# Kernel tuning notes

Hardware: AMD Instinct MI355X
Metric: run time of the kernel (lower is better)

Reference implementation:

```python
import jax, jax.numpy as jnp
import numpy as np

N_NODES = 100000
N_EDGES = 1600000
NFEAT, NHID, NCLASS = 64, 128, 32


def _glorot(key, shape):
    fan_in, fan_out = shape[0], shape[1]
    lim = np.sqrt(6.0 / (fan_in + fan_out))
    return jax.random.uniform(key, shape, jnp.float32, -lim, lim)


def setup_inputs() -> dict:
    key = jax.random.key(0)
    ks = jax.random.split(key, 12)
    x = jax.random.normal(ks[0], (N_NODES, NFEAT), jnp.float32)
    edge_idx = jax.random.randint(ks[1], (2, N_EDGES), 0, N_NODES, jnp.int64)
    edge_weight = jax.random.uniform(ks[2], (N_EDGES,), jnp.float32)
    return {
        "x": x,
        "edge_idx": edge_idx,
        "edge_weight": edge_weight,
        # SAGEConv 1: out = mean_agg(x) @ Wl1 + b1 + x @ Wr1
        "Wl1": _glorot(ks[3], (NFEAT, NHID)),
        "Wr1": _glorot(ks[4], (NFEAT, NHID)),
        "b1": jnp.zeros((NHID,), jnp.float32),
        # SAGEConv 2
        "Wl2": _glorot(ks[5], (NHID, NHID)),
        "Wr2": _glorot(ks[6], (NHID, NHID)),
        "b2": jnp.zeros((NHID,), jnp.float32),
        # fc head: Linear(nhid, nclass) -> Linear(nclass, 1)
        "Wfc1": _glorot(ks[7], (NHID, NCLASS)),
        "bfc1": jnp.zeros((NCLASS,), jnp.float32),
        "Wfc2": _glorot(ks[8], (NCLASS, 1)),
        "bfc2": jnp.zeros((1,), jnp.float32),
    }


def _sage_conv(x, src, dst, Wl, Wr, b, n_nodes):
    # mean aggregation of source features at destination nodes
    msg_sum = jax.ops.segment_sum(x[src], dst, num_segments=n_nodes)  # [N, d]
    deg = jax.ops.segment_sum(jnp.ones((src.shape[0], 1), x.dtype), dst,
                              num_segments=n_nodes)                    # [N, 1]
    mean = msg_sum / jnp.maximum(deg, 1.0)
    return mean @ Wl + b + x @ Wr


def reference(x, edge_idx, edge_weight, Wl1, Wr1, b1, Wl2, Wr2, b2,
              Wfc1, bfc1, Wfc2, bfc2):
    n_nodes = x.shape[0]
    src, dst = edge_idx[0], edge_idx[1]
    # dropout is identity in eval mode (training=False)
    h = _sage_conv(x, src, dst, Wl1, Wr1, b1, n_nodes)   # [N, nhid]
    h = _sage_conv(h, src, dst, Wl2, Wr2, b2, n_nodes)   # [N, nhid]
    h = h @ Wfc1 + bfc1                                   # [N, nclass]
    out = h @ Wfc2 + bfc2                                 # [N, 1]
    return out
```

## Files before the change

kernel.cpp:

```cpp
#include <hip/hip_runtime.h>

#define S_NODES 512
#define S_SHIFT 9
#define CAP     10240
#define CHUNK   8192

__global__ void weights_kernel(const float* __restrict__ Wl1, const float* __restrict__ Wr1,
                               const float* __restrict__ b1,
                               const float* __restrict__ Wl2, const float* __restrict__ Wr2,
                               const float* __restrict__ b2,
                               const float* __restrict__ Wfc1, const float* __restrict__ bfc1,
                               const float* __restrict__ Wfc2, const float* __restrict__ bfc2,
                               float* __restrict__ wbuf) {
    __shared__ float u[128], vl2[128], vr2[128], w2[32];
    int t = threadIdx.x;
    if (t < 32) w2[t] = Wfc2[t];
    __syncthreads();
    {
        float s = 0.f;
        for (int k = 0; k < 32; ++k) s += Wfc1[t * 32 + k] * w2[k];
        u[t] = s;
    }
    __syncthreads();
    {
        float a = 0.f, b = 0.f;
        for (int k = 0; k < 128; ++k) {
            a += Wl2[t * 128 + k] * u[k];
            b += Wr2[t * 128 + k] * u[k];
        }
        vl2[t] = a; vr2[t] = b;
    }
    __syncthreads();
    if (t < 64) {
        float wa = 0.f, wb = 0.f, wc = 0.f;
        for (int j = 0; j < 128; ++j) {
            float l1 = Wl1[t * 128 + j], r1 = Wr1[t * 128 + j];
            wc += l1 * vl2[j];
            wb += l1 * vr2[j] + r1 * vl2[j];
            wa += r1 * vr2[j];
        }
        wbuf[t] = wa; wbuf[64 + t] = wb; wbuf[128 + t] = wc;
    }
    if (t == 0) {
        float c0 = bfc2[0], c1 = 0.f;
        for (int j = 0; j < 128; ++j) {
            c0 += b1[j] * vr2[j] + b2[j] * u[j];
            c1 += b1[j] * vl2[j];
        }
        for (int k = 0; k < 32; ++k) c0 += bfc1[k] * w2[k];
        wbuf[192] = c0; wbuf[193] = c1;
    }
}

__global__ void dots_kernel(const float* __restrict__ x, const float* __restrict__ wbuf,
                            float* __restrict__ ga, float2* __restrict__ gbc, int N) {
    int tid = threadIdx.x, lane = tid & 63;
    int node = blockIdx.x * 4 + (tid >> 6);
    if (node >= N) return;
    float v = x[(size_t)node * 64 + lane];
    float a = v * wbuf[lane];
    float b = v * wbuf[64 + lane];
    float c = v * wbuf[128 + lane];
    for (int off = 32; off > 0; off >>= 1) {
        a += __shfl_down(a, off);
        b += __shfl_down(b, off);
        c += __shfl_down(c, off);
    }
    if (lane == 0) { ga[node] = a; gbc[node] = make_float2(b, c); }
}

__global__ void scatter_bucket_kernel(const int* __restrict__ src, const int* __restrict__ dst,
                                      int E, int B, int* __restrict__ cursor,
                                      unsigned* __restrict__ bucket) {
    __shared__ unsigned pk[CHUNK];
    __shared__ unsigned char bn[CHUNK];
    __shared__ int hist[256], lbase[256], lcur[256];
    int t = threadIdx.x;
    int e0 = blockIdx.x * CHUNK;
    int cnt = E - e0; if (cnt > CHUNK) cnt = CHUNK;
    hist[t] = 0; lcur[t] = 0;
    __syncthreads();
    for (int i = t; i < cnt; i += 256) {
        int s = src[e0 + i], d = dst[e0 + i];
        int b = d >> S_SHIFT;
        pk[i] = ((unsigned)s << S_SHIFT) | (unsigned)(d & (S_NODES - 1));
        bn[i] = (unsigned char)b;
        atomicAdd(&hist[b], 1);
    }
    __syncthreads();
    if (t < B && hist[t] > 0) lbase[t] = atomicAdd(&cursor[t], hist[t]);
    __syncthreads();
    for (int i = t; i < cnt; i += 256) {
        int b = bn[i];
        int off = atomicAdd(&lcur[b], 1);
        bucket[(size_t)b * CAP + (unsigned)(lbase[b] + off)] = pk[i];
    }
}

__global__ void aggA_kernel(const unsigned* __restrict__ bucket, const int* __restrict__ cursor,
                            const float2* __restrict__ gbc, const float* __restrict__ ga,
                            const float* __restrict__ wbuf,
                            float* __restrict__ q, float* __restrict__ t1,
                            float* __restrict__ inv, int N) {
    __shared__ float aB[S_NODES], aC[S_NODES];
    __shared__ int cnt[S_NODES];
    int t = threadIdx.x, b = blockIdx.x;
    for (int i = t; i < S_NODES; i += 256) { aB[i] = 0.f; aC[i] = 0.f; cnt[i] = 0; }
    __syncthreads();
    int n = cursor[b];
    const unsigned* bp = bucket + (size_t)b * CAP;
    for (int i = t; i < n; i += 256) {
        unsigned u = bp[i];
        float2 g = gbc[u >> S_SHIFT];
        int dl = u & (S_NODES - 1);
        atomicAdd(&aB[dl], g.x);
        atomicAdd(&aC[dl], g.y);
        atomicAdd(&cnt[dl], 1);
    }
    __syncthreads();
    float c0 = wbuf[192], c1 = wbuf[193];
    int base = b << S_SHIFT;
    for (int i = t; i < S_NODES; i += 256) {
        int node = base + i;
        if (node < N) {
            int d = cnt[i];
            float iv = 1.0f / ((d > 0) ? (float)d : 1.0f);
            inv[node] = iv;
            q[node]   = iv * aC[i];
            t1[node]  = ga[node] + iv * aB[i] + c0 + (d > 0 ? c1 : 0.f);
        }
    }
}

__global__ void aggB_kernel(const unsigned* __restrict__ bucket, const int* __restrict__ cursor,
                            const float* __restrict__ q, const float* __restrict__ t1,
                            const float* __restrict__ inv, float* __restrict__ out, int N) {
    __shared__ float a2[S_NODES];
    int t = threadIdx.x, b = blockIdx.x;
    for (int i = t; i < S_NODES; i += 256) a2[i] = 0.f;
    __syncthreads();
    int n = cursor[b];
    const unsigned* bp = bucket + (size_t)b * CAP;
    for (int i = t; i < n; i += 256) {
        unsigned u = bp[i];
        atomicAdd(&a2[u & (S_NODES - 1)], q[u >> S_SHIFT]);
    }
    __syncthreads();
    int base = b << S_SHIFT;
    for (int i = t; i < S_NODES; i += 256) {
        int node = base + i;
        if (node < N) out[node] = t1[node] + inv[node] * a2[i];
    }
}

extern "C" void kernel_launch(void* const* d_in, const int* in_sizes, int n_in,
                              void* d_out, int out_size, void* d_ws, size_t ws_size,
                              hipStream_t stream) {
    const float* x    = (const float*)d_in[0];
    const int*   eidx = (const int*)d_in[1];
    const float* Wl1  = (const float*)d_in[3];
    const float* Wr1  = (const float*)d_in[4];
    const float* b1   = (const float*)d_in[5];
    const float* Wl2  = (const float*)d_in[6];
    const float* Wr2  = (const float*)d_in[7];
    const float* b2   = (const float*)d_in[8];
    const float* Wfc1 = (const float*)d_in[9];
    const float* bfc1 = (const float*)d_in[10];
    const float* Wfc2 = (const float*)d_in[11];
    const float* bfc2 = (const float*)d_in[12];

    const int N = in_sizes[0] / 64;
    const int E = in_sizes[2];
    const int* src = eidx;
    const int* dst = eidx + E;
    const int B = (N + S_NODES - 1) / S_NODES;

    char* ws = (char*)d_ws;
    int*      cursor = (int*)(ws);
    float*    wbuf   = (float*)(ws + 1024);
    float*    ga     = (float*)(ws + 2048);
    float*    q      = (float*)(ws + 2048 + (size_t)N * 4);
    float*    t1     = (float*)(ws + 2048 + (size_t)N * 8);
    float*    inv    = (float*)(ws + 2048 + (size_t)N * 12);
    float2*   gbc    = (float2*)(ws + 2048 + (size_t)N * 16);
    unsigned* bucket = (unsigned*)(ws + 2048 + (size_t)N * 24);

    hipMemsetAsync(cursor, 0, 1024, stream);

    weights_kernel<<<1, 128, 0, stream>>>(Wl1, Wr1, b1, Wl2, Wr2, b2,
                                          Wfc1, bfc1, Wfc2, bfc2, wbuf);

    dots_kernel<<<(N + 3) / 4, 256, 0, stream>>>(x, wbuf, ga, gbc, N);

    scatter_bucket_kernel<<<(E + CHUNK - 1) / CHUNK, 256, 0, stream>>>(src, dst, E, B,
                                                                       cursor, bucket);

    aggA_kernel<<<B, 256, 0, stream>>>(bucket, cursor, gbc, ga, wbuf, q, t1, inv, N);
    aggB_kernel<<<B, 256, 0, stream>>>(bucket, cursor, q, t1, inv, (float*)d_out, N);
}
```

Baseline: 193.2 us.

## Fuse weight folding, node dots and edge bucketing into one heterogeneous kernel

Merges the weight-collapse, per-node dot-product and edge-scatter kernels into one launch. Some blocks bucket edges while the rest each recompute the folded weight vectors redundantly and then do the dots with a grid-stride loop. This removes two launches and the serial dependency on the single-block weight kernel. The aggregation kernels move to 1024 threads per block to raise parallelism per bucket, and the scatter uses 512 threads. The cost is redundant weight computation in 192 blocks and larger blocks competing for resources.

Result: no change. 196.2 us (+1.5%).

```diff
diff --git a/kernel.cpp b/kernel.cpp
--- a/kernel.cpp
+++ b/kernel.cpp
@@ -4,152 +4,154 @@
 #define S_SHIFT 9
 #define CAP     10240
 #define CHUNK   8192
-
-__global__ void weights_kernel(const float* __restrict__ Wl1, const float* __restrict__ Wr1,
-                               const float* __restrict__ b1,
-                               const float* __restrict__ Wl2, const float* __restrict__ Wr2,
-                               const float* __restrict__ b2,
-                               const float* __restrict__ Wfc1, const float* __restrict__ bfc1,
-                               const float* __restrict__ Wfc2, const float* __restrict__ bfc2,
-                               float* __restrict__ wbuf) {
-    __shared__ float u[128], vl2[128], vr2[128], w2[32];
-    int t = threadIdx.x;
-    if (t < 32) w2[t] = Wfc2[t];
-    __syncthreads();
-    {
-        float s = 0.f;
-        for (int k = 0; k < 32; ++k) s += Wfc1[t * 32 + k] * w2[k];
-        u[t] = s;
-    }
-    __syncthreads();
-    {
-        float a = 0.f, b = 0.f;
-        for (int k = 0; k < 128; ++k) {
-            a += Wl2[t * 128 + k] * u[k];
-            b += Wr2[t * 128 + k] * u[k];
-        }
-        vl2[t] = a; vr2[t] = b;
-    }
-    __syncthreads();
-    if (t < 64) {
-        float wa = 0.f, wb = 0.f, wc = 0.f;
-        for (int j = 0; j < 128; ++j) {
-            float l1 = Wl1[t * 128 + j], r1 = Wr1[t * 128 + j];
-            wc += l1 * vl2[j];
-            wb += l1 * vr2[j] + r1 * vl2[j];
-            wa += r1 * vr2[j];
-        }
-        wbuf[t] = wa; wbuf[64 + t] = wb; wbuf[128 + t] = wc;
-    }
-    if (t == 0) {
-        float c0 = bfc2[0], c1 = 0.f;
-        for (int j = 0; j < 128; ++j) {
-            c0 += b1[j] * vr2[j] + b2[j] * u[j];
-            c1 += b1[j] * vl2[j];
-        }
-        for (int k = 0; k < 32; ++k) c0 += bfc1[k] * w2[k];
-        wbuf[192] = c0; wbuf[193] = c1;
-    }
-}
-
-__global__ void dots_kernel(const float* __restrict__ x, const float* __restrict__ wbuf,
-                            float* __restrict__ ga, float2* __restrict__ gbc, int N) {
-    int tid = threadIdx.x, lane = tid & 63;
-    int node = blockIdx.x * 4 + (tid >> 6);
-    if (node >= N) return;
-    float v = x[(size_t)node * 64 + lane];
-    float a = v * wbuf[lane];
-    float b = v * wbuf[64 + lane];
-    float c = v * wbuf[128 + lane];
-    for (int off = 32; off > 0; off >>= 1) {
-        a += __shfl_down(a, off);
-        b += __shfl_down(b, off);
-        c += __shfl_down(c, off);
-    }
-    if (lane == 0) { ga[node] = a; gbc[node] = make_float2(b, c); }
-}
-
-__global__ void scatter_bucket_kernel(const int* __restrict__ src, const int* __restrict__ dst,
-                                      int E, int B, int* __restrict__ cursor,
-                                      unsigned* __restrict__ bucket) {
+#define FTH     512
+#define NDOTS   192
+
+__global__ __launch_bounds__(512) void fused_kernel(
+    const float* __restrict__ x,
+    const int* __restrict__ src, const int* __restrict__ dst, int E, int B, int nscat,
+    int* __restrict__ cursor, unsigned* __restrict__ bucket,
+    const float* __restrict__ Wl1, const float* __restrict__ Wr1, const float* __restrict__ b1,
+    const float* __restrict__ Wl2, const float* __restrict__ Wr2, const float* __restrict__ b2,
+    const float* __restrict__ Wfc1, const float* __restrict__ bfc1,
+    const float* __restrict__ Wfc2, const float* __restrict__ bfc2,
+    float* __restrict__ ga, float2* __restrict__ gbc, float* __restrict__ c01, int N)
+{
     __shared__ unsigned pk[CHUNK];
     __shared__ unsigned char bn[CHUNK];
     __shared__ int hist[256], lbase[256], lcur[256];
+    __shared__ float u[128], vl2[128], vr2[128], w2[32], wv[192];
+
     int t = threadIdx.x;
-    int e0 = blockIdx.x * CHUNK;
-    int cnt = E - e0; if (cnt > CHUNK) cnt = CHUNK;
-    hist[t] = 0; lcur[t] = 0;
-    __syncthreads();
-    for (int i = t; i < cnt; i += 256) {
-        int s = src[e0 + i], d = dst[e0 + i];
-        int b = d >> S_SHIFT;
-        pk[i] = ((unsigned)s << S_SHIFT) | (unsigned)(d & (S_NODES - 1));
-        bn[i] = (unsigned char)b;
-        atomicAdd(&hist[b], 1);
-    }
-    __syncthreads();
-    if (t < B && hist[t] > 0) lbase[t] = atomicAdd(&cursor[t], hist[t]);
-    __syncthreads();
-    for (int i = t; i < cnt; i += 256) {
-        int b = bn[i];
-        int off = atomicAdd(&lcur[b], 1);
-        bucket[(size_t)b * CAP + (unsigned)(lbase[b] + off)] = pk[i];
-    }
-}
-
-__global__ void aggA_kernel(const unsigned* __restrict__ bucket, const int* __restrict__ cursor,
-                            const float2* __restrict__ gbc, const float* __restrict__ ga,
-                            const float* __restrict__ wbuf,
-                            float* __restrict__ q, float* __restrict__ t1,
-                            float* __restrict__ inv, int N) {
+    if ((int)blockIdx.x < nscat) {
+        int e0 = blockIdx.x * CHUNK;
+        int cnt = E - e0; if (cnt > CHUNK) cnt = CHUNK;
+        if (t < 256) { hist[t] = 0; lcur[t] = 0; }
+        __syncthreads();
+        for (int i = t; i < cnt; i += FTH) {
+            int s = src[e0 + i], d = dst[e0 + i];
+            int b = d >> S_SHIFT;
+            pk[i] = ((unsigned)s << S_SHIFT) | (unsigned)(d & (S_NODES - 1));
+            bn[i] = (unsigned char)b;
+            atomicAdd(&hist[b], 1);
+        }
+        __syncthreads();
+        if (t < B && hist[t] > 0) lbase[t] = atomicAdd(&cursor[t], hist[t]);
+        __syncthreads();
+        for (int i = t; i < cnt; i += FTH) {
+            int b = bn[i];
+            int off = atomicAdd(&lcur[b], 1);
+            bucket[(size_t)b * CAP + (unsigned)(lbase[b] + off)] = pk[i];
+        }
+    } else {
+        if (t < 32) w2[t] = Wfc2[t];
+        __syncthreads();
+        if (t < 128) {
+            float s = 0.f;
+            for (int k = 0; k < 32; ++k) s += Wfc1[t * 32 + k] * w2[k];
+            u[t] = s;
+        }
+        __syncthreads();
+        if (t < 128) {
+            float a = 0.f, b = 0.f;
+            for (int k = 0; k < 128; ++k) {
+                a += Wl2[t * 128 + k] * u[k];
+                b += Wr2[t * 128 + k] * u[k];
+            }
+            vl2[t] = a; vr2[t] = b;
+        }
+        __syncthreads();
+        if (t < 64) {
+            float wa = 0.f, wb = 0.f, wc = 0.f;
+            for (int j = 0; j < 128; ++j) {
+                float l1 = Wl1[t * 128 + j], r1 = Wr1[t * 128 + j];
+                wc += l1 * vl2[j];
+                wb += l1 * vr2[j] + r1 * vl2[j];
+                wa += r1 * vr2[j];
+            }
+            wv[t] = wa; wv[64 + t] = wb; wv[128 + t] = wc;
+        }
+        if ((int)blockIdx.x == nscat && t == 0) {
+            float c0 = bfc2[0], c1 = 0.f;
+            for (int j = 0; j < 128; ++j) {
+                c0 += b1[j] * vr2[j] + b2[j] * u[j];
+                c1 += b1[j] * vl2[j];
+            }
+            for (int k = 0; k < 32; ++k) c0 += bfc1[k] * w2[k];
+            c01[0] = c0; c01[1] = c1;
+        }
+        __syncthreads();
+        int lane = t & 63, sub = t >> 6;
+        float wa = wv[lane], wb = wv[64 + lane], wc = wv[128 + lane];
+        int ngroups = (N + 7) / 8;
+        for (int g = (int)blockIdx.x - nscat; g < ngroups; g += NDOTS) {
+            int node = g * 8 + sub;
+            if (node >= N) continue;
+            float v = x[(size_t)node * 64 + lane];
+            float a = v * wa, b = v * wb, c = v * wc;
+            for (int off = 32; off > 0; off >>= 1) {
+                a += __shfl_down(a, off);
+                b += __shfl_down(b, off);
+                c += __shfl_down(c, off);
+            }
+            if (lane == 0) { ga[node] = a; gbc[node] = make_float2(b, c); }
+        }
+    }
+}
+
+__global__ __launch_bounds__(1024) void aggA_kernel(
+    const unsigned* __restrict__ bucket, const int* __restrict__ cursor,
+    const float2* __restrict__ gbc, const float* __restrict__ ga,
+    const float* __restrict__ c01,
+    float* __restrict__ q, float* __restrict__ t1, float* __restrict__ inv, int N)
+{
     __shared__ float aB[S_NODES], aC[S_NODES];
     __shared__ int cnt[S_NODES];
     int t = threadIdx.x, b = blockIdx.x;
-    for (int i = t; i < S_NODES; i += 256) { aB[i] = 0.f; aC[i] = 0.f; cnt[i] = 0; }
+    if (t < S_NODES) { aB[t] = 0.f; aC[t] = 0.f; cnt[t] = 0; }
     __syncthreads();
     int n = cursor[b];
     const unsigned* bp = bucket + (size_t)b * CAP;
-    for (int i = t; i < n; i += 256) {
-        unsigned u = bp[i];
-        float2 g = gbc[u >> S_SHIFT];
-        int dl = u & (S_NODES - 1);
+    for (int i = t; i < n; i += 1024) {
+        unsigned uu = bp[i];
+        float2 g = gbc[uu >> S_SHIFT];
+        int dl = uu & (S_NODES - 1);
         atomicAdd(&aB[dl], g.x);
         atomicAdd(&aC[dl], g.y);
         atomicAdd(&cnt[dl], 1);
     }
     __syncthreads();
-    float c0 = wbuf[192], c1 = wbuf[193];
-    int base = b << S_SHIFT;
-    for (int i = t; i < S_NODES; i += 256) {
-        int node = base + i;
+    if (t < S_NODES) {
+        int node = (b << S_SHIFT) + t;
         if (node < N) {
-            int d = cnt[i];
+            int d = cnt[t];
             float iv = 1.0f / ((d > 0) ? (float)d : 1.0f);
             inv[node] = iv;
-            q[node]   = iv * aC[i];
-            t1[node]  = ga[node] + iv * aB[i] + c0 + (d > 0 ? c1 : 0.f);
-        }
-    }
-}
-
-__global__ void aggB_kernel(const unsigned* __restrict__ bucket, const int* __restrict__ cursor,
-                            const float* __restrict__ q, const float* __restrict__ t1,
-                            const float* __restrict__ inv, float* __restrict__ out, int N) {
+            q[node]   = iv * aC[t];
+            t1[node]  = ga[node] + iv * aB[t] + c01[0] + (d > 0 ? c01[1] : 0.f);
+        }
+    }
+}
+
+__global__ __launch_bounds__(1024) void aggB_kernel(
+    const unsigned* __restrict__ bucket, const int* __restrict__ cursor,
+    const float* __restrict__ q, const float* __restrict__ t1,
+    const float* __restrict__ inv, float* __restrict__ out, int N)
+{
     __shared__ float a2[S_NODES];
     int t = threadIdx.x, b = blockIdx.x;
-    for (int i = t; i < S_NODES; i += 256) a2[i] = 0.f;
+    if (t < S_NODES) a2[t] = 0.f;
     __syncthreads();
     int n = cursor[b];
     const unsigned* bp = bucket + (size_t)b * CAP;
-    for (int i = t; i < n; i += 256) {
-        unsigned u = bp[i];
-        atomicAdd(&a2[u & (S_NODES - 1)], q[u >> S_SHIFT]);
-    }
-    __syncthreads();
-    int base = b << S_SHIFT;
-    for (int i = t; i < S_NODES; i += 256) {
-        int node = base + i;
-        if (node < N) out[node] = t1[node] + inv[node] * a2[i];
+    for (int i = t; i < n; i += 1024) {
+        unsigned uu = bp[i];
+        atomicAdd(&a2[uu & (S_NODES - 1)], q[uu >> S_SHIFT]);
+    }
+    __syncthreads();
+    if (t < S_NODES) {
+        int node = (b << S_SHIFT) + t;
+        if (node < N) out[node] = t1[node] + inv[node] * a2[t];
     }
 }
 
@@ -174,10 +176,11 @@
     const int* src = eidx;
     const int* dst = eidx + E;
     const int B = (N + S_NODES - 1) / S_NODES;
+    const int nscat = (E + CHUNK - 1) / CHUNK;
 
     char* ws = (char*)d_ws;
     int*      cursor = (int*)(ws);
-    float*    wbuf   = (float*)(ws + 1024);
+    float*    c01    = (float*)(ws + 1024);
     float*    ga     = (float*)(ws + 2048);
     float*    q      = (float*)(ws + 2048 + (size_t)N * 4);
     float*    t1     = (float*)(ws + 2048 + (size_t)N * 8);
@@ -187,14 +190,11 @@
 
     hipMemsetAsync(cursor, 0, 1024, stream);
 
-    weights_kernel<<<1, 128, 0, stream>>>(Wl1, Wr1, b1, Wl2, Wr2, b2,
-                                          Wfc1, bfc1, Wfc2, bfc2, wbuf);
-
-    dots_kernel<<<(N + 3) / 4, 256, 0, stream>>>(x, wbuf, ga, gbc, N);
-
-    scatter_bucket_kernel<<<(E + CHUNK - 1) / CHUNK, 256, 0, stream>>>(src, dst, E, B,
-                                                                       cursor, bucket);
-
-    aggA_kernel<<<B, 256, 0, stream>>>(bucket, cursor, gbc, ga, wbuf, q, t1, inv, N);
-    aggB_kernel<<<B, 256, 0, stream>>>(bucket, cursor, q, t1, inv, (float*)d_out, N);
-}
+    fused_kernel<<<nscat + NDOTS, FTH, 0, stream>>>(
+        x, src, dst, E, B, nscat, cursor, bucket,
+        Wl1, Wr1, b1, Wl2, Wr2, b2, Wfc1, bfc1, Wfc2, bfc2,
+        ga, gbc, c01, N);
+
+    aggA_kernel<<<B, 1024, 0, stream>>>(bucket, cursor, gbc, ga, c01, q, t1, inv, N);
+    aggB_kernel<<<B, 1024, 0, stream>>>(bucket, cursor, q, t1, inv, (float*)d_out, N);
+}
```
